# Optimization experiments

Measured on AMD Instinct MI355X. Metric: run time of the kernel, lower is better.

The kernel has to match this reference:

```python
import jax, jax.numpy as jnp
import numpy as np

N = 1_000_000   # total points
C = 20          # semantic classes
B = 4           # scenes in batch
L = 200         # instance label vocabulary
INST = 64       # number of proposals/instances
M = 300_000     # masked points (len(object_idxs))
T = 320_000     # total proposal rows
IGNORE = -100
PREPARE_EPOCHS = 128


def setup_inputs() -> dict:
    key = jax.random.key(0)
    ks = jax.random.split(key, 12)
    semantic_scores = jax.random.normal(ks[0], (N, C), jnp.float32)
    semantic_labels = jax.random.randint(ks[1], (N,), 0, C)
    lab = jax.random.randint(ks[2], (N,), 0, L)
    ign = jax.random.uniform(ks[3], (N,)) < 0.05
    instance_labels = jnp.where(ign, IGNORE, lab)
    pt_offsets = jax.random.normal(ks[4], (N, 3), jnp.float32)
    instance_info = jax.random.normal(ks[5], (N, 9), jnp.float32)
    coords = jax.random.normal(ks[6], (N, 3), jnp.float32)
    mask_logits = jax.random.normal(ks[7], (INST, M), jnp.float32)
    object_idxs = jax.random.randint(ks[8], (M,), 0, N)
    col1 = jax.random.randint(ks[9], (T,), 0, N)
    proposals_idx_shift = jnp.stack([jnp.zeros_like(col1), col1], axis=1)
    mids = jnp.sort(jax.random.randint(ks[10], (INST - 1,), 0, T))
    proposals_offset_shift = jnp.concatenate(
        [jnp.zeros((1,), jnp.int32), mids.astype(jnp.int32), jnp.full((1,), T, jnp.int32)])
    inst_batch_ids = jax.random.randint(ks[11], (INST,), 0, B)
    batch_offsets = jnp.array([0, N // 4, N // 2, 3 * N // 4, N], dtype=jnp.int32)
    batch_ids = jnp.clip(jnp.searchsorted(batch_offsets, object_idxs, side='right') - 1, 0, B - 1)
    inst_pred_seg_label = jax.random.randint(jax.random.fold_in(key, 99), (INST,), 0, C)
    return dict(semantic_scores=semantic_scores, pt_offsets=pt_offsets,
                instance_info=instance_info, coords=coords, mask_logits=mask_logits,
                semantic_labels=semantic_labels, instance_labels=instance_labels,
                object_idxs=object_idxs, proposals_idx_shift=proposals_idx_shift,
                proposals_offset_shift=proposals_offset_shift, inst_batch_ids=inst_batch_ids,
                batch_ids=batch_ids, batch_offsets=batch_offsets,
                inst_pred_seg_label=inst_pred_seg_label, epoch=200)


def reference(semantic_scores, pt_offsets, instance_info, coords, mask_logits,
              semantic_labels, instance_labels, object_idxs, proposals_idx_shift,
              proposals_offset_shift, inst_batch_ids, batch_ids, batch_offsets,
              inst_pred_seg_label, epoch):
    f32 = jnp.float32
    n_pts = semantic_scores.shape[0]
    n_inst, m_pts = mask_logits.shape
    n_batch = batch_offsets.shape[0] - 1
    LW = L + 1  # label buckets, bucket 0 == ignore(-100)

    # --- semantic cross entropy (ignore_index) ---
    logp = jax.nn.log_softmax(semantic_scores, axis=-1)
    sem_valid = semantic_labels != IGNORE
    safe_lab = jnp.where(sem_valid, semantic_labels, 0)
    nll = -jnp.take_along_axis(logp, safe_lab[:, None], axis=1)[:, 0]
    semantic_loss = jnp.sum(nll * sem_valid) / jnp.maximum(jnp.sum(sem_valid), 1)

    # --- offset losses ---
    gt_offsets = instance_info[:, 0:3] - coords
    pt_dist = jnp.sum(jnp.abs(pt_offsets - gt_offsets), axis=-1)
    valid = (instance_labels != IGNORE).astype(f32)
    vsum = jnp.sum(valid) + 1e-6
    offset_norm_loss = jnp.sum(pt_dist * valid) / vsum
    gt_u = gt_offsets / (jnp.linalg.norm(gt_offsets, axis=1, keepdims=True) + 1e-8)
    pt_u = pt_offsets / (jnp.linalg.norm(pt_offsets, axis=1, keepdims=True) + 1e-8)
    offset_dir_loss = jnp.sum(-jnp.sum(gt_u * pt_u, axis=-1) * valid) / vsum

    loss = semantic_loss + offset_norm_loss + offset_dir_loss

    if epoch > PREPARE_EPOCHS:
        # map instance labels to ids: ignore -> 0, label l -> l+1 (order-preserving, so
        # argmax-first tie-break == torch.mode smallest-value tie-break)
        labels_id = jnp.where(instance_labels == IGNORE, 0, instance_labels + 1)
        # segment id per proposal row from CSR offsets
        seg = jnp.clip(jnp.searchsorted(proposals_offset_shift, jnp.arange(T), side='right') - 1,
                       0, n_inst - 1)
        prop_lab = labels_id[proposals_idx_shift[:, 1]]
        hist = jax.ops.segment_sum(jnp.ones((T,), f32), seg * LW + prop_lab,
                                   num_segments=n_inst * LW).reshape(n_inst, LW)
        mode_id = jnp.argmax(hist, axis=1)                       # [INST] per-instance mode vote

        masked_lab = labels_id[object_idxs]                      # [M]
        sem_masked = semantic_labels[object_idxs]                # [M]
        skip = (mode_id == 0) | (inst_pred_seg_label <= 3)       # [INST]

        batch_match = inst_batch_ids[:, None] == batch_ids[None, :]           # [INST,M]
        sem_match = inst_pred_seg_label[:, None] == sem_masked[None, :]       # [INST,M]
        weights = batch_match.astype(f32) * jnp.where(skip[:, None], 1.0,
                                                      sem_match.astype(f32))  # [INST,M]

        # per-batch label histograms (full points and masked points)
        point_batch = jnp.clip(jnp.searchsorted(batch_offsets, jnp.arange(n_pts),
                                                side='right') - 1, 0, n_batch - 1)
        hist_full = jax.ops.segment_sum(jnp.ones((n_pts,), f32), point_batch * LW + labels_id,
                                        num_segments=n_batch * LW).reshape(n_batch, LW)
        hist_mask = jax.ops.segment_sum(jnp.ones((m_pts,), f32), batch_ids * LW + masked_lab,
                                        num_segments=n_batch * LW).reshape(n_batch, LW)
        num = hist_mask[inst_batch_ids, mode_id]
        den = hist_full[inst_batch_ids, mode_id]
        cover = jnp.where(den > 0, num / den, 0.0)
        pos = (~skip) & (cover > 0.3)
        inst_gt_mask = (pos[:, None] & (masked_lab[None, :] == mode_id[:, None])).astype(f32)

        pred = jax.nn.sigmoid(mask_logits)
        wb = (weights > 0).astype(f32)
        inter = jnp.sum(wb * pred * inst_gt_mask, axis=1)
        union = jnp.sum(wb * pred * pred, axis=1) + jnp.sum(wb * inst_gt_mask * inst_gt_mask, axis=1) + 1e-5
        dice_n = 1.0 - 2.0 * inter / union
        dice_valid = (~skip) & (jnp.sum(wb, axis=1) > 0)
        dice_loss = jnp.sum(jnp.where(dice_valid, dice_n, 0.0)) / (jnp.sum(dice_valid.astype(f32)) + 1e-6)

        # BCE(sigmoid(x), t) in stable form: softplus(x) - t*x
        bce = jax.nn.softplus(mask_logits) - inst_gt_mask * mask_logits
        score_loss = jnp.sum(bce * weights) / (jnp.sum(weights) + 1e-6)

        loss = loss + score_loss + dice_loss
    return loss
```

## Files before the change

### kernel.cpp

```cpp
#include <hip/hip_runtime.h>
#include <math.h>

namespace {

constexpr int N_PTS  = 1000000;
constexpr int C_CLS  = 20;
constexpr int N_B    = 4;
constexpr int L_LAB  = 200;
constexpr int LW     = L_LAB + 1;
constexpr int N_INST = 64;
constexpr int M_PTS  = 300000;
constexpr int T_PROP = 320000;
constexpr int IGN    = -100;
constexpr int PREP   = 128;

constexpr size_t OFF_G      = 0;
constexpr size_t OFF_INTER  = 64;
constexpr size_t OFF_UP     = 576;
constexpr size_t OFF_UG     = 1088;
constexpr size_t OFF_WBS    = 1600;
constexpr size_t OFF_SN     = 2112;
constexpr size_t OFF_HFULL  = 2624;
constexpr size_t OFF_HMASK  = 5840;
constexpr size_t OFF_IHIST  = 9056;
constexpr size_t OFF_FLAGS  = 60512;
constexpr size_t ZERO_BYTES = 60768;
constexpr size_t OFF_PART   = 60800;
constexpr size_t PART_BYTES = 5 * 1024 * 4;
constexpr size_t WS_PART_REQ = OFF_PART + PART_BYTES;
constexpr size_t OFF_META   = WS_PART_REQ;
constexpr size_t WS_REQUIRED = OFF_META + (size_t)M_PTS * 2;

__device__ __forceinline__ float waveSumF(float v) {
  #pragma unroll
  for (int off = 32; off > 0; off >>= 1) v += __shfl_down(v, off, 64);
  return v;
}
__device__ __forceinline__ int waveMaxI(int v) {
  #pragma unroll
  for (int off = 32; off > 0; off >>= 1) v = max(v, __shfl_down(v, off, 64));
  return v;
}

constexpr int PB_PT   = 1024;
constexpr int PB_HF   = 256;
constexpr int PB_PROP = 256;
constexpr int PB_HM   = 256;
constexpr int A_BLOCKS = PB_PT + PB_HF + PB_PROP + PB_HM;

constexpr int WREG = 560;

__global__ __launch_bounds__(256) void k_A(const float* __restrict__ scores,
                                           const float* __restrict__ pt_off,
                                           const float* __restrict__ info,
                                           const float* __restrict__ coords,
                                           const int* __restrict__ sem_lab,
                                           const int* __restrict__ inst_lab,
                                           const int* __restrict__ obj_idx,
                                           const int* __restrict__ batch_ids,
                                           const int* __restrict__ prop_idx,
                                           const int* __restrict__ prop_off,
                                           const int* __restrict__ batch_off,
                                           double* __restrict__ g,
                                           float* __restrict__ part,
                                           int use_part,
                                           int* __restrict__ hist_full,
                                           int* __restrict__ hist_mask,
                                           int* __restrict__ inst_hist,
                                           unsigned short* __restrict__ meta,
                                           int write_meta) {
  __shared__ float4 shbuf4[4 * WREG];
  int*   sh  = reinterpret_cast<int*>(shbuf4);
  float* shf = reinterpret_cast<float*>(shbuf4);
  const int bx = blockIdx.x;

  if (bx < PB_PT) {
    const int lane = threadIdx.x & 63, wv = threadIdx.x >> 6;
    float4* shw4 = shbuf4 + wv * WREG;
    float*  shwf = reinterpret_cast<float*>(shw4);
    float s_nll = 0.f, s_cnt = 0.f, s_dist = 0.f, s_dir = 0.f, s_val = 0.f;

    constexpr int NT      = N_PTS / 64;
    constexpr int TSTRIDE = PB_PT * 4;
    const int base = bx * 4 + wv;
    const int nit = (NT - bx * 4 + TSTRIDE - 1) / TSTRIDE;

    for (int it = 0; it < nit; ++it) {
      const int tile = base + it * TSTRIDE;
      if (tile < NT) {
        const int p = tile * 64 + lane;
        const int sl = sem_lab[p];
        const int il = inst_lab[p];

        const float4* s4 = reinterpret_cast<const float4*>(scores) + (size_t)tile * 320;
        #pragma unroll
        for (int r = 0; r < 5; ++r) shw4[r * 64 + lane] = s4[r * 64 + lane];
        const float4* c4 = reinterpret_cast<const float4*>(coords) + (size_t)tile * 48;
        const float4* o4 = reinterpret_cast<const float4*>(pt_off) + (size_t)tile * 48;
        const float4* i4 = reinterpret_cast<const float4*>(info)   + (size_t)tile * 144;
        if (lane < 48) { shw4[320 + lane] = c4[lane]; shw4[368 + lane] = o4[lane]; }
        shw4[416 + lane] = i4[lane];
        shw4[480 + lane] = i4[64 + lane];
        if (lane < 16) shw4[544 + lane] = i4[128 + lane];

        float mx = -3.4e38f;
        #pragma unroll
        for (int r = 0; r < 5; ++r) {
          const float4 a = shw4[lane * 5 + r];
          mx = fmaxf(mx, fmaxf(fmaxf(a.x, a.y), fmaxf(a.z, a.w)));
        }
        float se = 0.f;
        #pragma unroll
        for (int r = 0; r < 5; ++r) {
          const float4 a = shw4[lane * 5 + r];
          se += __expf(a.x - mx) + __expf(a.y - mx) + __expf(a.z - mx) + __expf(a.w - mx);
        }
        const float xs = shwf[lane * 20 + ((sl == IGN) ? 0 : sl)];
        if (sl != IGN) { s_nll += (mx + __logf(se)) - xs; s_cnt += 1.f; }

        if (il != IGN) {
          const float cx = shwf[1280 + 3 * lane + 0];
          const float cy = shwf[1280 + 3 * lane + 1];
          const float cz = shwf[1280 + 3 * lane + 2];
          const float ox = shwf[1472 + 3 * lane + 0];
          const float oy = shwf[1472 + 3 * lane + 1];
          const float oz = shwf[1472 + 3 * lane + 2];
          const float gx = shwf[1664 + 9 * lane + 0] - cx;
          const float gy = shwf[1664 + 9 * lane + 1] - cy;
          const float gz = shwf[1664 + 9 * lane + 2] - cz;
          s_val  += 1.f;
          s_dist += fabsf(ox - gx) + fabsf(oy - gy) + fabsf(oz - gz);
          const float gn = sqrtf(gx * gx + gy * gy + gz * gz) + 1e-8f;
          const float pn = sqrtf(ox * ox + oy * oy + oz * oz) + 1e-8f;
          s_dir += -((gx * ox + gy * oy + gz * oz) / (gn * pn));
        }
      }
    }

    __syncthreads();
    float vals[5] = { s_nll, s_cnt, s_dist, s_dir, s_val };
    #pragma unroll
    for (int k = 0; k < 5; ++k) {
      const float t = waveSumF(vals[k]);
      if (lane == 0) shf[k * 4 + wv] = t;
    }
    __syncthreads();
    if (threadIdx.x < 5) {
      const float s = shf[threadIdx.x * 4 + 0] + shf[threadIdx.x * 4 + 1] +
                      shf[threadIdx.x * 4 + 2] + shf[threadIdx.x * 4 + 3];
      if (use_part) part[threadIdx.x * PB_PT + bx] = s;
      else          atomicAdd(&g[threadIdx.x], (double)s);
    }
  } else if (bx < PB_PT + PB_HF) {
    for (int t = threadIdx.x; t < N_B * LW; t += blockDim.x) sh[t] = 0;
    __syncthreads();
    const int b1 = batch_off[1], b2 = batch_off[2], b3 = batch_off[3];
    const int blk = bx - PB_PT;
    const int4* il4p = reinterpret_cast<const int4*>(inst_lab);
    const int nq = N_PTS / 4;
    for (int q = blk * blockDim.x + threadIdx.x; q < nq; q += PB_HF * blockDim.x) {
      const int4 v = il4p[q];
      const int p = q * 4;
      const int ils[4] = { v.x, v.y, v.z, v.w };
      #pragma unroll
      for (int k = 0; k < 4; ++k) {
        const int lab = (ils[k] == IGN) ? 0 : (ils[k] + 1);
        const int pp = p + k;
        int pb = 0;
        if (pp >= b1) pb = 1;
        if (pp >= b2) pb = 2;
        if (pp >= b3) pb = 3;
        atomicAdd(&sh[pb * LW + lab], 1);
      }
    }
    __syncthreads();
    for (int t = threadIdx.x; t < N_B * LW; t += blockDim.x)
      if (sh[t]) atomicAdd(&hist_full[t], sh[t]);
  } else if (bx < PB_PT + PB_HF + PB_PROP) {
    if (threadIdx.x <= N_INST) sh[threadIdx.x] = prop_off[threadIdx.x];
    __syncthreads();
    const int blk = bx - PB_PT - PB_HF;
    const int4* pi4 = reinterpret_cast<const int4*>(prop_idx);
    const int nq = T_PROP / 2;
    for (int q = blk * blockDim.x + threadIdx.x; q < nq; q += PB_PROP * blockDim.x) {
      const int4 v = pi4[q];
      const int t0 = 2 * q, t1 = 2 * q + 1;
      const int il0 = inst_lab[v.y];
      const int il1 = inst_lab[v.w];
      int lo0 = 0, hi0 = N_INST + 1, lo1 = 0, hi1 = N_INST + 1;
      #pragma unroll
      for (int s = 0; s < 7; ++s) {
        const int m0 = (lo0 + hi0) >> 1;
        if (m0 <= N_INST && sh[m0] <= t0) lo0 = m0 + 1; else hi0 = m0;
        const int m1 = (lo1 + hi1) >> 1;
        if (m1 <= N_INST && sh[m1] <= t1) lo1 = m1 + 1; else hi1 = m1;
      }
      const int seg0 = min(lo0 - 1, N_INST - 1);
      const int seg1 = min(lo1 - 1, N_INST - 1);
      const int lab0 = (il0 == IGN) ? 0 : (il0 + 1);
      const int lab1 = (il1 == IGN) ? 0 : (il1 + 1);
      atomicAdd(&inst_hist[seg0 * LW + lab0], 1);
      atomicAdd(&inst_hist[seg1 * LW + lab1], 1);
    }
  } else {
    for (int t = threadIdx.x; t < N_B * LW; t += blockDim.x) sh[t] = 0;
    __syncthreads();
    const int blk = bx - PB_PT - PB_HF - PB_PROP;
    const int4* oi4 = reinterpret_cast<const int4*>(obj_idx);
    const int4* bi4 = reinterpret_cast<const int4*>(batch_ids);
    ushort4* m4 = reinterpret_cast<ushort4*>(meta);
    const int nq = M_PTS / 4;
    for (int q = blk * blockDim.x + threadIdx.x; q < nq; q += PB_HM * blockDim.x) {
      const int4 o = oi4[q];
      const int4 b = bi4[q];
      const int il0 = inst_lab[o.x], il1 = inst_lab[o.y],
                il2 = inst_lab[o.z], il3 = inst_lab[o.w];
      const int sm0 = sem_lab[o.x], sm1 = sem_lab[o.y],
                sm2 = sem_lab[o.z], sm3 = sem_lab[o.w];
      const int ml0 = (il0 == IGN) ? 0 : (il0 + 1);
      const int ml1 = (il1 == IGN) ? 0 : (il1 + 1);
      const int ml2 = (il2 == IGN) ? 0 : (il2 + 1);
      const int ml3 = (il3 == IGN) ? 0 : (il3 + 1);
      atomicAdd(&sh[b.x * LW + ml0], 1);
      atomicAdd(&sh[b.y * LW + ml1], 1);
      atomicAdd(&sh[b.z * LW + ml2], 1);
      atomicAdd(&sh[b.w * LW + ml3], 1);
      if (write_meta) {
        ushort4 mm;
        mm.x = (unsigned short)(ml0 | (sm0 << 8) | (b.x << 13));
        mm.y = (unsigned short)(ml1 | (sm1 << 8) | (b.y << 13));
        mm.z = (unsigned short)(ml2 | (sm2 << 8) | (b.z << 13));
        mm.w = (unsigned short)(ml3 | (sm3 << 8) | (b.w << 13));
        m4[q] = mm;
      }
    }
    __syncthreads();
    for (int t = threadIdx.x; t < N_B * LW; t += blockDim.x)
      if (sh[t]) atomicAdd(&hist_mask[t], sh[t]);
  }
}

__global__ __launch_bounds__(256) void k_argmax(const int* __restrict__ inst_hist,
                                                const int* __restrict__ hist_full,
                                                const int* __restrict__ hist_mask,
                                                const int* __restrict__ inst_batch_ids,
                                                const int* __restrict__ inst_seg,
                                                int* __restrict__ flags) {
  __shared__ int red[4];
  const int i = blockIdx.x;
  const int t = threadIdx.x;
  int key = 0;
  if (t < LW) {
    const int cnt = inst_hist[i * LW + t];
    key = (cnt << 8) | (255 - t);
  }
  key = waveMaxI(key);
  const int lane = t & 63, wv = t >> 6;
  if (lane == 0) red[wv] = key;
  __syncthreads();
  if (t == 0) {
    int k = max(max(red[0], red[1]), max(red[2], red[3]));
    const int m = 255 - (k & 0xFF);
    const int b = inst_batch_ids[i];
    const int seg = inst_seg[i];
    const bool skip = (m == 0) || (seg <= 3);
    const float num = (float)hist_mask[b * LW + m];
    const float den = (float)hist_full[b * LW + m];
    const float cover = (den > 0.f) ? (num / den) : 0.f;
    const bool pos = (!skip) && (cover > 0.3f);
    flags[i] = m | (skip ? 0x100 : 0) | (pos ? 0x200 : 0) | (b << 10) | (seg << 12);
  }
}

template <bool USE_META>
__global__ __launch_bounds__(256) void k_mask(const float* __restrict__ logits,
                                              const unsigned short* __restrict__ meta,
                                              const int* __restrict__ obj_idx,
                                              const int* __restrict__ inst_lab,
                                              const int* __restrict__ sem_lab,
                                              const int* __restrict__ batch_ids,
                                              const int* __restrict__ flags,
                                              double* __restrict__ i_inter,
                                              double* __restrict__ i_up,
                                              double* __restrict__ i_ug,
                                              double* __restrict__ i_wbs,
                                              double* __restrict__ i_sn) {
  const int i  = blockIdx.y;
  const int fl = flags[i];
  const int  mode_i = fl & 0xFF;
  const bool skip   = (fl >> 8) & 1;
  const bool pos    = (fl >> 9) & 1;
  const int  bi     = (fl >> 10) & 3;
  const int  seg    = (fl >> 12) & 31;

  float inter = 0.f, up = 0.f, ug = 0.f, wbs = 0.f, sn = 0.f;

  if (USE_META) {
    const float4* row4 = reinterpret_cast<const float4*>(logits + (size_t)i * M_PTS);
    const ushort4* m4  = reinterpret_cast<const ushort4*>(meta);
    const int nq = M_PTS / 4;
    for (int q = blockIdx.x * blockDim.x + threadIdx.x; q < nq; q += gridDim.x * blockDim.x) {
      const float4  x4 = row4[q];
      const ushort4 d4 = m4[q];
      const float xs[4] = { x4.x, x4.y, x4.z, x4.w };
      const int   ds[4] = { d4.x, d4.y, d4.z, d4.w };
      #pragma unroll
      for (int k = 0; k < 4; ++k) {
        const int md = ds[k];
        const int ml = md & 0xFF;
        const int sm = (md >> 8) & 31;
        const int b  = (md >> 13) & 3;
        const bool w  = (b == bi) && (skip || (sm == seg));
        const bool gt = pos && (ml == mode_i);
        const float x  = xs[k];
        const float e  = __expf(-fabsf(x));
        const float r  = __builtin_amdgcn_rcpf(1.f + e);
        const float pr = (x >= 0.f) ? r : e * r;
        const float sp = fmaxf(x, 0.f) + __logf(1.f + e);
        const float wf = w ? 1.f : 0.f;
        const float gf = gt ? 1.f : 0.f;
        up    += wf * pr * pr;
        wbs   += wf;
        sn    += wf * (sp - gf * x);
        inter += wf * gf * pr;
        ug    += wf * gf;
      }
    }
  } else {
    const float* row = logits + (size_t)i * M_PTS;
    for (int j = blockIdx.x * blockDim.x + threadIdx.x; j < M_PTS; j += gridDim.x * blockDim.x) {
      const int o  = obj_idx[j];
      const int il = inst_lab[o];
      const int ml = (il == IGN) ? 0 : (il + 1);
      const int sm = sem_lab[o];
      const int b  = batch_ids[j];
      const bool w  = (b == bi) && (skip || (sm == seg));
      const bool gt = pos && (ml == mode_i);
      const float x  = row[j];
      const float e  = __expf(-fabsf(x));
      const float r  = __builtin_amdgcn_rcpf(1.f + e);
      const float pr = (x >= 0.f) ? r : e * r;
      const float sp = fmaxf(x, 0.f) + __logf(1.f + e);
      const float wf = w ? 1.f : 0.f;
      const float gf = gt ? 1.f : 0.f;
      up    += wf * pr * pr;
      wbs   += wf;
      sn    += wf * (sp - gf * x);
      inter += wf * gf * pr;
      ug    += wf * gf;
    }
  }

  __shared__ float red[5][4];
  float vals[5] = { inter, up, ug, wbs, sn };
  const int lane = threadIdx.x & 63, wv = threadIdx.x >> 6;
  #pragma unroll
  for (int k = 0; k < 5; ++k) {
    const float t = waveSumF(vals[k]);
    if (lane == 0) red[k][wv] = t;
  }
  __syncthreads();
  if (threadIdx.x < 5) {
    const float s = red[threadIdx.x][0] + red[threadIdx.x][1] + red[threadIdx.x][2] + red[threadIdx.x][3];
    double* dst = (threadIdx.x == 0) ? (i_inter + i)
                : (threadIdx.x == 1) ? (i_up + i)
                : (threadIdx.x == 2) ? (i_ug + i)
                : (threadIdx.x == 3) ? (i_wbs + i)
                                     : (i_sn + i);
    atomicAdd(dst, (double)s);
  }
}

__global__ __launch_bounds__(256) void k_final(const double* __restrict__ g,
                                               const float* __restrict__ part,
                                               int use_part,
                                               const double* __restrict__ i_inter,
                                               const double* __restrict__ i_up,
                                               const double* __restrict__ i_ug,
                                               const double* __restrict__ i_wbs,
                                               const double* __restrict__ i_sn,
                                               const int* __restrict__ flags,
                                               const int* __restrict__ epoch,
                                               float* __restrict__ out) {
  __shared__ double sred[5][4];
  __shared__ double sG[5];
  __shared__ double sI[4];
  const int t = threadIdx.x, lane = t & 63, wv = t >> 6;

  if (use_part) {
    #pragma unroll
    for (int c = 0; c < 5; ++c) {
      double v = 0.0;
      #pragma unroll
      for (int j = 0; j < 4; ++j) v += (double)part[c * 1024 + t + j * 256];
      #pragma unroll
      for (int off = 32; off > 0; off >>= 1) v += __shfl_down(v, off, 64);
      if (lane == 0) sred[c][wv] = v;
    }
    __syncthreads();
    if (t < 5) sG[t] = sred[t][0] + sred[t][1] + sred[t][2] + sred[t][3];
  } else {
    if (t < 5) sG[t] = g[t];
  }

  const bool act = epoch[0] > PREP;
  if (t < 64) {
    double sn = 0.0, wsum = 0.0, dice = 0.0, dcnt = 0.0;
    if (act) {
      wsum = i_wbs[t];
      sn   = i_sn[t];
      const bool skip = (flags[t] >> 8) & 1;
      if (!skip && wsum > 0.0) {
        const double un = i_up[t] + i_ug[t] + 1e-5;
        dice = 1.0 - 2.0 * i_inter[t] / un;
        dcnt = 1.0;
      }
      #pragma unroll
      for (int off = 32; off > 0; off >>= 1) {
        wsum += __shfl_down(wsum, off, 64);
        sn   += __shfl_down(sn,   off, 64);
        dice += __shfl_down(dice, off, 64);
        dcnt += __shfl_down(dcnt, off, 64);
      }
    }
    if (t == 0) { sI[0] = sn; sI[1] = wsum; sI[2] = dice; sI[3] = dcnt; }
  }
  __syncthreads();
  if (t == 0) {
    double loss = sG[0] / fmax(sG[1], 1.0);
    const double vsum = sG[4] + 1e-6;
    loss += sG[2] / vsum + sG[3] / vsum;
    if (act) loss += sI[0] / (sI[1] + 1e-6) + sI[2] / (sI[3] + 1e-6);
    out[0] = (float)loss;
  }
}

}

extern "C" void kernel_launch(void* const* d_in, const int* in_sizes, int n_in,
                              void* d_out, int out_size, void* d_ws, size_t ws_size,
                              hipStream_t stream) {
  const float* semantic_scores  = (const float*)d_in[0];
  const float* pt_offsets       = (const float*)d_in[1];
  const float* instance_info    = (const float*)d_in[2];
  const float* coords           = (const float*)d_in[3];
  const float* mask_logits      = (const float*)d_in[4];
  const int*   semantic_labels  = (const int*)d_in[5];
  const int*   instance_labels  = (const int*)d_in[6];
  const int*   object_idxs      = (const int*)d_in[7];
  const int*   proposals_idx    = (const int*)d_in[8];
  const int*   proposals_off    = (const int*)d_in[9];
  const int*   inst_batch_ids   = (const int*)d_in[10];
  const int*   batch_ids        = (const int*)d_in[11];
  const int*   batch_offsets    = (const int*)d_in[12];
  const int*   inst_seg         = (const int*)d_in[13];
  const int*   epoch            = (const int*)d_in[14];
  float* out = (float*)d_out;

  char* w = (char*)d_ws;
  double* g        = (double*)(w + OFF_G);
  double* i_inter  = (double*)(w + OFF_INTER);
  double* i_up     = (double*)(w + OFF_UP);
  double* i_ug     = (double*)(w + OFF_UG);
  double* i_wbs    = (double*)(w + OFF_WBS);
  double* i_sn     = (double*)(w + OFF_SN);
  int* hist_full   = (int*)(w + OFF_HFULL);
  int* hist_mask   = (int*)(w + OFF_HMASK);
  int* inst_hist   = (int*)(w + OFF_IHIST);
  int* flags       = (int*)(w + OFF_FLAGS);
  float* part      = (float*)(w + OFF_PART);
  unsigned short* meta = (unsigned short*)(w + OFF_META);

  const bool use_part = (ws_size >= WS_PART_REQ);
  const bool use_meta = (ws_size >= WS_REQUIRED);

  (void)hipMemsetAsync(d_ws, 0, ZERO_BYTES, stream);

  k_A<<<A_BLOCKS, 256, 0, stream>>>(semantic_scores, pt_offsets, instance_info, coords,
                                    semantic_labels, instance_labels, object_idxs,
                                    batch_ids, proposals_idx, proposals_off, batch_offsets,
                                    g, part, use_part ? 1 : 0,
                                    hist_full, hist_mask, inst_hist, meta,
                                    use_meta ? 1 : 0);

  k_argmax<<<N_INST, 256, 0, stream>>>(inst_hist, hist_full, hist_mask,
                                       inst_batch_ids, inst_seg, flags);

  dim3 mgrid(40, N_INST);
  if (use_meta) {
    k_mask<true><<<mgrid, 256, 0, stream>>>(mask_logits, meta, object_idxs, instance_labels,
                                            semantic_labels, batch_ids, flags,
                                            i_inter, i_up, i_ug, i_wbs, i_sn);
  } else {
    k_mask<false><<<mgrid, 256, 0, stream>>>(mask_logits, meta, object_idxs, instance_labels,
                                             semantic_labels, batch_ids, flags,
                                             i_inter, i_up, i_ug, i_wbs, i_sn);
  }
  k_final<<<1, 256, 0, stream>>>(g, part, use_part ? 1 : 0,
                                 i_inter, i_up, i_ug, i_wbs, i_sn, flags, epoch, out);
}
```

Measured before the change: 293.4 us.

## Software-prefetch point tiles into registers and unroll mask-row loads by two

```diff
diff --git a/kernel.cpp b/kernel.cpp
--- a/kernel.cpp
+++ b/kernel.cpp
@@ -42,39 +42,72 @@
   return v;
 }
 
-constexpr int PB_PT   = 1024;
 constexpr int PB_HF   = 256;
 constexpr int PB_PROP = 256;
 constexpr int PB_HM   = 256;
-constexpr int A_BLOCKS = PB_PT + PB_HF + PB_PROP + PB_HM;
+constexpr int PB_PT   = 1024;
+constexpr int PT_BASE = PB_HF + PB_PROP + PB_HM;
+constexpr int A_BLOCKS = PT_BASE + PB_PT;
 
 constexpr int WREG = 560;
 
-__global__ __launch_bounds__(256) void k_A(const float* __restrict__ scores,
-                                           const float* __restrict__ pt_off,
-                                           const float* __restrict__ info,
-                                           const float* __restrict__ coords,
-                                           const int* __restrict__ sem_lab,
-                                           const int* __restrict__ inst_lab,
-                                           const int* __restrict__ obj_idx,
-                                           const int* __restrict__ batch_ids,
-                                           const int* __restrict__ prop_idx,
-                                           const int* __restrict__ prop_off,
-                                           const int* __restrict__ batch_off,
-                                           double* __restrict__ g,
-                                           float* __restrict__ part,
-                                           int use_part,
-                                           int* __restrict__ hist_full,
-                                           int* __restrict__ hist_mask,
-                                           int* __restrict__ inst_hist,
-                                           unsigned short* __restrict__ meta,
-                                           int write_meta) {
+struct PtRegs {
+  float4 r0, r1, r2, r3, r4;
+  float4 rc, ro;
+  float4 ri0, ri1, ri2;
+  int sl, il;
+};
+
+__device__ __forceinline__ void pt_load(PtRegs& R, int tile, int lane,
+                                        const float4* __restrict__ s4b,
+                                        const float4* __restrict__ c4b,
+                                        const float4* __restrict__ o4b,
+                                        const float4* __restrict__ i4b,
+                                        const int* __restrict__ sem_lab,
+                                        const int* __restrict__ inst_lab) {
+  const float4* s4 = s4b + (size_t)tile * 320;
+  R.r0 = s4[lane];
+  R.r1 = s4[64 + lane];
+  R.r2 = s4[128 + lane];
+  R.r3 = s4[192 + lane];
+  R.r4 = s4[256 + lane];
+  const float4* c4 = c4b + (size_t)tile * 48;
+  const float4* o4 = o4b + (size_t)tile * 48;
+  const float4* i4 = i4b + (size_t)tile * 144;
+  if (lane < 48) { R.rc = c4[lane]; R.ro = o4[lane]; }
+  R.ri0 = i4[lane];
+  R.ri1 = i4[64 + lane];
+  if (lane < 16) R.ri2 = i4[128 + lane];
+  const int p = tile * 64 + lane;
+  R.sl = sem_lab[p];
+  R.il = inst_lab[p];
+}
+
+__global__ __launch_bounds__(256, 4) void k_A(const float* __restrict__ scores,
+                                              const float* __restrict__ pt_off,
+                                              const float* __restrict__ info,
+                                              const float* __restrict__ coords,
+                                              const int* __restrict__ sem_lab,
+                                              const int* __restrict__ inst_lab,
+                                              const int* __restrict__ obj_idx,
+                                              const int* __restrict__ batch_ids,
+                                              const int* __restrict__ prop_idx,
+                                              const int* __restrict__ prop_off,
+                                              const int* __restrict__ batch_off,
+                                              double* __restrict__ g,
+                                              float* __restrict__ part,
+                                              int use_part,
+                                              int* __restrict__ hist_full,
+                                              int* __restrict__ hist_mask,
+                                              int* __restrict__ inst_hist,
+                                              unsigned short* __restrict__ meta,
+                                              int write_meta) {
   __shared__ float4 shbuf4[4 * WREG];
   int*   sh  = reinterpret_cast<int*>(shbuf4);
   float* shf = reinterpret_cast<float*>(shbuf4);
   const int bx = blockIdx.x;
 
-  if (bx < PB_PT) {
+  if (bx >= PT_BASE) {
     const int lane = threadIdx.x & 63, wv = threadIdx.x >> 6;
     float4* shw4 = shbuf4 + wv * WREG;
     float*  shwf = reinterpret_cast<float*>(shw4);
@@ -82,27 +115,39 @@
 
     constexpr int NT      = N_PTS / 64;
     constexpr int TSTRIDE = PB_PT * 4;
-    const int base = bx * 4 + wv;
-    const int nit = (NT - bx * 4 + TSTRIDE - 1) / TSTRIDE;
+    const int bxp  = bx - PT_BASE;
+    const int base = bxp * 4 + wv;
+    const int nit  = (NT - bxp * 4 + TSTRIDE - 1) / TSTRIDE;
+
+    const float4* s4b = reinterpret_cast<const float4*>(scores);
+    const float4* c4b = reinterpret_cast<const float4*>(coords);
+    const float4* o4b = reinterpret_cast<const float4*>(pt_off);
+    const float4* i4b = reinterpret_cast<const float4*>(info);
+
+    PtRegs R;
+    int tile = base;
+    if (tile < NT) pt_load(R, tile, lane, s4b, c4b, o4b, i4b, sem_lab, inst_lab);
 
     for (int it = 0; it < nit; ++it) {
-      const int tile = base + it * TSTRIDE;
-      if (tile < NT) {
-        const int p = tile * 64 + lane;
-        const int sl = sem_lab[p];
-        const int il = inst_lab[p];
-
-        const float4* s4 = reinterpret_cast<const float4*>(scores) + (size_t)tile * 320;
-        #pragma unroll
-        for (int r = 0; r < 5; ++r) shw4[r * 64 + lane] = s4[r * 64 + lane];
-        const float4* c4 = reinterpret_cast<const float4*>(coords) + (size_t)tile * 48;
-        const float4* o4 = reinterpret_cast<const float4*>(pt_off) + (size_t)tile * 48;
-        const float4* i4 = reinterpret_cast<const float4*>(info)   + (size_t)tile * 144;
-        if (lane < 48) { shw4[320 + lane] = c4[lane]; shw4[368 + lane] = o4[lane]; }
-        shw4[416 + lane] = i4[lane];
-        shw4[480 + lane] = i4[64 + lane];
-        if (lane < 16) shw4[544 + lane] = i4[128 + lane];
-
+      const int cur = tile;
+      const int nxt = tile + TSTRIDE;
+      const int sl = R.sl, il = R.il;
+
+      if (cur < NT) {
+        shw4[lane]        = R.r0;
+        shw4[64 + lane]   = R.r1;
+        shw4[128 + lane]  = R.r2;
+        shw4[192 + lane]  = R.r3;
+        shw4[256 + lane]  = R.r4;
+        if (lane < 48) { shw4[320 + lane] = R.rc; shw4[368 + lane] = R.ro; }
+        shw4[416 + lane]  = R.ri0;
+        shw4[480 + lane]  = R.ri1;
+        if (lane < 16) shw4[544 + lane] = R.ri2;
+      }
+
+      if (nxt < NT) pt_load(R, nxt, lane, s4b, c4b, o4b, i4b, sem_lab, inst_lab);
+
+      if (cur < NT) {
         float mx = -3.4e38f;
         #pragma unroll
         for (int r = 0; r < 5; ++r) {
@@ -135,6 +180,7 @@
           s_dir += -((gx * ox + gy * oy + gz * oz) / (gn * pn));
         }
       }
+      tile = nxt;
     }
 
     __syncthreads();
@@ -148,14 +194,14 @@
     if (threadIdx.x < 5) {
       const float s = shf[threadIdx.x * 4 + 0] + shf[threadIdx.x * 4 + 1] +
                       shf[threadIdx.x * 4 + 2] + shf[threadIdx.x * 4 + 3];
-      if (use_part) part[threadIdx.x * PB_PT + bx] = s;
+      if (use_part) part[threadIdx.x * PB_PT + bxp] = s;
       else          atomicAdd(&g[threadIdx.x], (double)s);
     }
-  } else if (bx < PB_PT + PB_HF) {
+  } else if (bx < PB_HF) {
     for (int t = threadIdx.x; t < N_B * LW; t += blockDim.x) sh[t] = 0;
     __syncthreads();
     const int b1 = batch_off[1], b2 = batch_off[2], b3 = batch_off[3];
-    const int blk = bx - PB_PT;
+    const int blk = bx;
     const int4* il4p = reinterpret_cast<const int4*>(inst_lab);
     const int nq = N_PTS / 4;
     for (int q = blk * blockDim.x + threadIdx.x; q < nq; q += PB_HF * blockDim.x) {
@@ -176,10 +222,10 @@
     __syncthreads();
     for (int t = threadIdx.x; t < N_B * LW; t += blockDim.x)
       if (sh[t]) atomicAdd(&hist_full[t], sh[t]);
-  } else if (bx < PB_PT + PB_HF + PB_PROP) {
+  } else if (bx < PB_HF + PB_PROP) {
     if (threadIdx.x <= N_INST) sh[threadIdx.x] = prop_off[threadIdx.x];
     __syncthreads();
-    const int blk = bx - PB_PT - PB_HF;
+    const int blk = bx - PB_HF;
     const int4* pi4 = reinterpret_cast<const int4*>(prop_idx);
     const int nq = T_PROP / 2;
     for (int q = blk * blockDim.x + threadIdx.x; q < nq; q += PB_PROP * blockDim.x) {
@@ -205,7 +251,7 @@
   } else {
     for (int t = threadIdx.x; t < N_B * LW; t += blockDim.x) sh[t] = 0;
     __syncthreads();
-    const int blk = bx - PB_PT - PB_HF - PB_PROP;
+    const int blk = bx - PB_HF - PB_PROP;
     const int4* oi4 = reinterpret_cast<const int4*>(obj_idx);
     const int4* bi4 = reinterpret_cast<const int4*>(batch_ids);
     ushort4* m4 = reinterpret_cast<ushort4*>(meta);
@@ -295,37 +341,47 @@
 
   float inter = 0.f, up = 0.f, ug = 0.f, wbs = 0.f, sn = 0.f;
 
+  auto acc4 = [&](const float4& x4, const ushort4& d4) {
+    const float xs[4] = { x4.x, x4.y, x4.z, x4.w };
+    const int   ds[4] = { d4.x, d4.y, d4.z, d4.w };
+    #pragma unroll
+    for (int k = 0; k < 4; ++k) {
+      const int md = ds[k];
+      const int ml = md & 0xFF;
+      const int sm = (md >> 8) & 31;
+      const int b  = (md >> 13) & 3;
+      const bool w  = (b == bi) && (skip || (sm == seg));
+      const bool gt = pos && (ml == mode_i);
+      const float x  = xs[k];
+      const float e  = __expf(-fabsf(x));
+      const float r  = __builtin_amdgcn_rcpf(1.f + e);
+      const float pr = (x >= 0.f) ? r : e * r;
+      const float sp = fmaxf(x, 0.f) + __logf(1.f + e);
+      const float wf = w ? 1.f : 0.f;
+      const float gf = gt ? 1.f : 0.f;
+      up    += wf * pr * pr;
+      wbs   += wf;
+      sn    += wf * (sp - gf * x);
+      inter += wf * gf * pr;
+      ug    += wf * gf;
+    }
+  };
+
   if (USE_META) {
     const float4* row4 = reinterpret_cast<const float4*>(logits + (size_t)i * M_PTS);
     const ushort4* m4  = reinterpret_cast<const ushort4*>(meta);
     const int nq = M_PTS / 4;
-    for (int q = blockIdx.x * blockDim.x + threadIdx.x; q < nq; q += gridDim.x * blockDim.x) {
-      const float4  x4 = row4[q];
-      const ushort4 d4 = m4[q];
-      const float xs[4] = { x4.x, x4.y, x4.z, x4.w };
-      const int   ds[4] = { d4.x, d4.y, d4.z, d4.w };
-      #pragma unroll
-      for (int k = 0; k < 4; ++k) {
-        const int md = ds[k];
-        const int ml = md & 0xFF;
-        const int sm = (md >> 8) & 31;
-        const int b  = (md >> 13) & 3;
-        const bool w  = (b == bi) && (skip || (sm == seg));
-        const bool gt = pos && (ml == mode_i);
-        const float x  = xs[k];
-        const float e  = __expf(-fabsf(x));
-        const float r  = __builtin_amdgcn_rcpf(1.f + e);
-        const float pr = (x >= 0.f) ? r : e * r;
-        const float sp = fmaxf(x, 0.f) + __logf(1.f + e);
-        const float wf = w ? 1.f : 0.f;
-        const float gf = gt ? 1.f : 0.f;
-        up    += wf * pr * pr;
-        wbs   += wf;
-        sn    += wf * (sp - gf * x);
-        inter += wf * gf * pr;
-        ug    += wf * gf;
-      }
-    }
+    const int stride = gridDim.x * blockDim.x;
+    int q = blockIdx.x * blockDim.x + threadIdx.x;
+    for (; q + stride < nq; q += 2 * stride) {
+      const float4  xa = row4[q];
+      const ushort4 da = m4[q];
+      const float4  xb = row4[q + stride];
+      const ushort4 db = m4[q + stride];
+      acc4(xa, da);
+      acc4(xb, db);
+    }
+    for (; q < nq; q += stride) acc4(row4[q], m4[q]);
   } else {
     const float* row = logits + (size_t)i * M_PTS;
     for (int j = blockIdx.x * blockDim.x + threadIdx.x; j < M_PTS; j += gridDim.x * blockDim.x) {
```

Result: slower. 317.5 us (+8.2%).

## Move point-loss pass into mask kernel and fold argmax into per-block prologue

Applied to the files above, without the earlier changes.

```diff
diff --git a/kernel.cpp b/kernel.cpp
--- a/kernel.cpp
+++ b/kernel.cpp
@@ -13,6 +13,19 @@
 constexpr int T_PROP = 320000;
 constexpr int IGN    = -100;
 constexpr int PREP   = 128;
+
+constexpr int GB_HF   = 256;
+constexpr int GB_PROP = 256;
+constexpr int GB_HM   = 256;
+constexpr int G_BLOCKS = GB_HF + GB_PROP + GB_HM;
+
+constexpr int JB_PT   = 2048;
+constexpr int JB_MK   = 2048;
+constexpr int J_BLOCKS = JB_PT + JB_MK;
+constexpr int NT       = N_PTS / 64;
+constexpr int PT_WAVES = JB_PT * 4;
+constexpr int MK_PER_I = JB_MK / N_INST;
+constexpr int MSTRIDE  = MK_PER_I * 256;
 
 constexpr size_t OFF_G      = 0;
 constexpr size_t OFF_INTER  = 64;
@@ -26,7 +39,7 @@
 constexpr size_t OFF_FLAGS  = 60512;
 constexpr size_t ZERO_BYTES = 60768;
 constexpr size_t OFF_PART   = 60800;
-constexpr size_t PART_BYTES = 5 * 1024 * 4;
+constexpr size_t PART_BYTES = 5 * (size_t)JB_PT * 4;
 constexpr size_t WS_PART_REQ = OFF_PART + PART_BYTES;
 constexpr size_t OFF_META   = WS_PART_REQ;
 constexpr size_t WS_REQUIRED = OFF_META + (size_t)M_PTS * 2;
@@ -42,123 +55,28 @@
   return v;
 }
 
-constexpr int PB_PT   = 1024;
-constexpr int PB_HF   = 256;
-constexpr int PB_PROP = 256;
-constexpr int PB_HM   = 256;
-constexpr int A_BLOCKS = PB_PT + PB_HF + PB_PROP + PB_HM;
-
-constexpr int WREG = 560;
-
-__global__ __launch_bounds__(256) void k_A(const float* __restrict__ scores,
-                                           const float* __restrict__ pt_off,
-                                           const float* __restrict__ info,
-                                           const float* __restrict__ coords,
-                                           const int* __restrict__ sem_lab,
-                                           const int* __restrict__ inst_lab,
-                                           const int* __restrict__ obj_idx,
-                                           const int* __restrict__ batch_ids,
-                                           const int* __restrict__ prop_idx,
-                                           const int* __restrict__ prop_off,
-                                           const int* __restrict__ batch_off,
-                                           double* __restrict__ g,
-                                           float* __restrict__ part,
-                                           int use_part,
-                                           int* __restrict__ hist_full,
-                                           int* __restrict__ hist_mask,
-                                           int* __restrict__ inst_hist,
-                                           unsigned short* __restrict__ meta,
-                                           int write_meta) {
-  __shared__ float4 shbuf4[4 * WREG];
-  int*   sh  = reinterpret_cast<int*>(shbuf4);
-  float* shf = reinterpret_cast<float*>(shbuf4);
+__global__ __launch_bounds__(256) void k_gather(const int* __restrict__ sem_lab,
+                                                const int* __restrict__ inst_lab,
+                                                const int* __restrict__ obj_idx,
+                                                const int* __restrict__ batch_ids,
+                                                const int* __restrict__ prop_idx,
+                                                const int* __restrict__ prop_off,
+                                                const int* __restrict__ batch_off,
+                                                int* __restrict__ hist_full,
+                                                int* __restrict__ hist_mask,
+                                                int* __restrict__ inst_hist,
+                                                unsigned short* __restrict__ meta,
+                                                int write_meta) {
+  __shared__ int sh[N_B * LW];
   const int bx = blockIdx.x;
 
-  if (bx < PB_PT) {
-    const int lane = threadIdx.x & 63, wv = threadIdx.x >> 6;
-    float4* shw4 = shbuf4 + wv * WREG;
-    float*  shwf = reinterpret_cast<float*>(shw4);
-    float s_nll = 0.f, s_cnt = 0.f, s_dist = 0.f, s_dir = 0.f, s_val = 0.f;
-
-    constexpr int NT      = N_PTS / 64;
-    constexpr int TSTRIDE = PB_PT * 4;
-    const int base = bx * 4 + wv;
-    const int nit = (NT - bx * 4 + TSTRIDE - 1) / TSTRIDE;
-
-    for (int it = 0; it < nit; ++it) {
-      const int tile = base + it * TSTRIDE;
-      if (tile < NT) {
-        const int p = tile * 64 + lane;
-        const int sl = sem_lab[p];
-        const int il = inst_lab[p];
-
-        const float4* s4 = reinterpret_cast<const float4*>(scores) + (size_t)tile * 320;
-        #pragma unroll
-        for (int r = 0; r < 5; ++r) shw4[r * 64 + lane] = s4[r * 64 + lane];
-        const float4* c4 = reinterpret_cast<const float4*>(coords) + (size_t)tile * 48;
-        const float4* o4 = reinterpret_cast<const float4*>(pt_off) + (size_t)tile * 48;
-        const float4* i4 = reinterpret_cast<const float4*>(info)   + (size_t)tile * 144;
-        if (lane < 48) { shw4[320 + lane] = c4[lane]; shw4[368 + lane] = o4[lane]; }
-        shw4[416 + lane] = i4[lane];
-        shw4[480 + lane] = i4[64 + lane];
-        if (lane < 16) shw4[544 + lane] = i4[128 + lane];
-
-        float mx = -3.4e38f;
-        #pragma unroll
-        for (int r = 0; r < 5; ++r) {
-          const float4 a = shw4[lane * 5 + r];
-          mx = fmaxf(mx, fmaxf(fmaxf(a.x, a.y), fmaxf(a.z, a.w)));
-        }
-        float se = 0.f;
-        #pragma unroll
-        for (int r = 0; r < 5; ++r) {
-          const float4 a = shw4[lane * 5 + r];
-          se += __expf(a.x - mx) + __expf(a.y - mx) + __expf(a.z - mx) + __expf(a.w - mx);
-        }
-        const float xs = shwf[lane * 20 + ((sl == IGN) ? 0 : sl)];
-        if (sl != IGN) { s_nll += (mx + __logf(se)) - xs; s_cnt += 1.f; }
-
-        if (il != IGN) {
-          const float cx = shwf[1280 + 3 * lane + 0];
-          const float cy = shwf[1280 + 3 * lane + 1];
-          const float cz = shwf[1280 + 3 * lane + 2];
-          const float ox = shwf[1472 + 3 * lane + 0];
-          const float oy = shwf[1472 + 3 * lane + 1];
-          const float oz = shwf[1472 + 3 * lane + 2];
-          const float gx = shwf[1664 + 9 * lane + 0] - cx;
-          const float gy = shwf[1664 + 9 * lane + 1] - cy;
-          const float gz = shwf[1664 + 9 * lane + 2] - cz;
-          s_val  += 1.f;
-          s_dist += fabsf(ox - gx) + fabsf(oy - gy) + fabsf(oz - gz);
-          const float gn = sqrtf(gx * gx + gy * gy + gz * gz) + 1e-8f;
-          const float pn = sqrtf(ox * ox + oy * oy + oz * oz) + 1e-8f;
-          s_dir += -((gx * ox + gy * oy + gz * oz) / (gn * pn));
-        }
-      }
-    }
-
-    __syncthreads();
-    float vals[5] = { s_nll, s_cnt, s_dist, s_dir, s_val };
-    #pragma unroll
-    for (int k = 0; k < 5; ++k) {
-      const float t = waveSumF(vals[k]);
-      if (lane == 0) shf[k * 4 + wv] = t;
-    }
-    __syncthreads();
-    if (threadIdx.x < 5) {
-      const float s = shf[threadIdx.x * 4 + 0] + shf[threadIdx.x * 4 + 1] +
-                      shf[threadIdx.x * 4 + 2] + shf[threadIdx.x * 4 + 3];
-      if (use_part) part[threadIdx.x * PB_PT + bx] = s;
-      else          atomicAdd(&g[threadIdx.x], (double)s);
-    }
-  } else if (bx < PB_PT + PB_HF) {
+  if (bx < GB_HF) {
     for (int t = threadIdx.x; t < N_B * LW; t += blockDim.x) sh[t] = 0;
     __syncthreads();
     const int b1 = batch_off[1], b2 = batch_off[2], b3 = batch_off[3];
-    const int blk = bx - PB_PT;
     const int4* il4p = reinterpret_cast<const int4*>(inst_lab);
     const int nq = N_PTS / 4;
-    for (int q = blk * blockDim.x + threadIdx.x; q < nq; q += PB_HF * blockDim.x) {
+    for (int q = bx * blockDim.x + threadIdx.x; q < nq; q += GB_HF * blockDim.x) {
       const int4 v = il4p[q];
       const int p = q * 4;
       const int ils[4] = { v.x, v.y, v.z, v.w };
@@ -176,13 +94,13 @@
     __syncthreads();
     for (int t = threadIdx.x; t < N_B * LW; t += blockDim.x)
       if (sh[t]) atomicAdd(&hist_full[t], sh[t]);
-  } else if (bx < PB_PT + PB_HF + PB_PROP) {
+  } else if (bx < GB_HF + GB_PROP) {
     if (threadIdx.x <= N_INST) sh[threadIdx.x] = prop_off[threadIdx.x];
     __syncthreads();
-    const int blk = bx - PB_PT - PB_HF;
+    const int blk = bx - GB_HF;
     const int4* pi4 = reinterpret_cast<const int4*>(prop_idx);
     const int nq = T_PROP / 2;
-    for (int q = blk * blockDim.x + threadIdx.x; q < nq; q += PB_PROP * blockDim.x) {
+    for (int q = blk * blockDim.x + threadIdx.x; q < nq; q += GB_PROP * blockDim.x) {
       const int4 v = pi4[q];
       const int t0 = 2 * q, t1 = 2 * q + 1;
       const int il0 = inst_lab[v.y];
@@ -205,12 +123,12 @@
   } else {
     for (int t = threadIdx.x; t < N_B * LW; t += blockDim.x) sh[t] = 0;
     __syncthreads();
-    const int blk = bx - PB_PT - PB_HF - PB_PROP;
+    const int blk = bx - GB_HF - GB_PROP;
     const int4* oi4 = reinterpret_cast<const int4*>(obj_idx);
     const int4* bi4 = reinterpret_cast<const int4*>(batch_ids);
     ushort4* m4 = reinterpret_cast<ushort4*>(meta);
     const int nq = M_PTS / 4;
-    for (int q = blk * blockDim.x + threadIdx.x; q < nq; q += PB_HM * blockDim.x) {
+    for (int q = blk * blockDim.x + threadIdx.x; q < nq; q += GB_HM * blockDim.x) {
       const int4 o = oi4[q];
       const int4 b = bi4[q];
       const int il0 = inst_lab[o.x], il1 = inst_lab[o.y],
@@ -240,79 +158,157 @@
   }
 }
 
-__global__ __launch_bounds__(256) void k_argmax(const int* __restrict__ inst_hist,
-                                                const int* __restrict__ hist_full,
-                                                const int* __restrict__ hist_mask,
-                                                const int* __restrict__ inst_batch_ids,
-                                                const int* __restrict__ inst_seg,
-                                                int* __restrict__ flags) {
-  __shared__ int red[4];
-  const int i = blockIdx.x;
-  const int t = threadIdx.x;
-  int key = 0;
-  if (t < LW) {
-    const int cnt = inst_hist[i * LW + t];
-    key = (cnt << 8) | (255 - t);
-  }
-  key = waveMaxI(key);
-  const int lane = t & 63, wv = t >> 6;
-  if (lane == 0) red[wv] = key;
-  __syncthreads();
-  if (t == 0) {
-    int k = max(max(red[0], red[1]), max(red[2], red[3]));
-    const int m = 255 - (k & 0xFF);
-    const int b = inst_batch_ids[i];
-    const int seg = inst_seg[i];
-    const bool skip = (m == 0) || (seg <= 3);
-    const float num = (float)hist_mask[b * LW + m];
-    const float den = (float)hist_full[b * LW + m];
-    const float cover = (den > 0.f) ? (num / den) : 0.f;
-    const bool pos = (!skip) && (cover > 0.3f);
-    flags[i] = m | (skip ? 0x100 : 0) | (pos ? 0x200 : 0) | (b << 10) | (seg << 12);
-  }
-}
-
 template <bool USE_META>
-__global__ __launch_bounds__(256) void k_mask(const float* __restrict__ logits,
-                                              const unsigned short* __restrict__ meta,
-                                              const int* __restrict__ obj_idx,
-                                              const int* __restrict__ inst_lab,
-                                              const int* __restrict__ sem_lab,
-                                              const int* __restrict__ batch_ids,
-                                              const int* __restrict__ flags,
-                                              double* __restrict__ i_inter,
-                                              double* __restrict__ i_up,
-                                              double* __restrict__ i_ug,
-                                              double* __restrict__ i_wbs,
-                                              double* __restrict__ i_sn) {
-  const int i  = blockIdx.y;
-  const int fl = flags[i];
-  const int  mode_i = fl & 0xFF;
-  const bool skip   = (fl >> 8) & 1;
-  const bool pos    = (fl >> 9) & 1;
-  const int  bi     = (fl >> 10) & 3;
-  const int  seg    = (fl >> 12) & 31;
-
-  float inter = 0.f, up = 0.f, ug = 0.f, wbs = 0.f, sn = 0.f;
-
-  if (USE_META) {
-    const float4* row4 = reinterpret_cast<const float4*>(logits + (size_t)i * M_PTS);
-    const ushort4* m4  = reinterpret_cast<const ushort4*>(meta);
-    const int nq = M_PTS / 4;
-    for (int q = blockIdx.x * blockDim.x + threadIdx.x; q < nq; q += gridDim.x * blockDim.x) {
-      const float4  x4 = row4[q];
-      const ushort4 d4 = m4[q];
-      const float xs[4] = { x4.x, x4.y, x4.z, x4.w };
-      const int   ds[4] = { d4.x, d4.y, d4.z, d4.w };
+__global__ __launch_bounds__(256, 8) void k_joint(const float* __restrict__ scores,
+                                                  const float* __restrict__ pt_off,
+                                                  const float* __restrict__ info,
+                                                  const float* __restrict__ coords,
+                                                  const int* __restrict__ sem_lab,
+                                                  const int* __restrict__ inst_lab,
+                                                  const int* __restrict__ obj_idx,
+                                                  const int* __restrict__ batch_ids,
+                                                  const float* __restrict__ logits,
+                                                  const unsigned short* __restrict__ meta,
+                                                  const int* __restrict__ inst_hist,
+                                                  const int* __restrict__ hist_full,
+                                                  const int* __restrict__ hist_mask,
+                                                  const int* __restrict__ inst_batch_ids,
+                                                  const int* __restrict__ inst_seg,
+                                                  int* __restrict__ flags,
+                                                  double* __restrict__ g,
+                                                  float* __restrict__ part,
+                                                  int use_part,
+                                                  double* __restrict__ i_inter,
+                                                  double* __restrict__ i_up,
+                                                  double* __restrict__ i_ug,
+                                                  double* __restrict__ i_wbs,
+                                                  double* __restrict__ i_sn) {
+  __shared__ float4 shbuf4[4 * 320];
+  float* shf = reinterpret_cast<float*>(shbuf4);
+  int*   shi = reinterpret_cast<int*>(shbuf4);
+  const int bx = blockIdx.x;
+  const int lane = threadIdx.x & 63, wv = threadIdx.x >> 6;
+
+  if (bx < JB_PT) {
+    float4* shw4 = shbuf4 + wv * 320;
+    float*  shwf = reinterpret_cast<float*>(shw4);
+    float s_nll = 0.f, s_cnt = 0.f, s_dist = 0.f, s_dir = 0.f, s_val = 0.f;
+
+    const int wgid = bx * 4 + wv;
+    const float4* s4b = reinterpret_cast<const float4*>(scores);
+    const float4* c4b = reinterpret_cast<const float4*>(coords);
+    const float4* o4b = reinterpret_cast<const float4*>(pt_off);
+    const float4* i4b = reinterpret_cast<const float4*>(info);
+
+    for (int tile = wgid; tile < NT; tile += PT_WAVES) {
+      const int p = tile * 64 + lane;
+      const int sl = sem_lab[p];
+      const int il = inst_lab[p];
+
+      const float4* s4 = s4b + (size_t)tile * 320;
+      #pragma unroll
+      for (int r = 0; r < 5; ++r) shw4[r * 64 + lane] = s4[r * 64 + lane];
+
+      float mx = -3.4e38f;
+      #pragma unroll
+      for (int r = 0; r < 5; ++r) {
+        const float4 a = shw4[lane * 5 + r];
+        mx = fmaxf(mx, fmaxf(fmaxf(a.x, a.y), fmaxf(a.z, a.w)));
+      }
+      float se = 0.f;
+      #pragma unroll
+      for (int r = 0; r < 5; ++r) {
+        const float4 a = shw4[lane * 5 + r];
+        se += __expf(a.x - mx) + __expf(a.y - mx) + __expf(a.z - mx) + __expf(a.w - mx);
+      }
+      const float xs = shwf[lane * 20 + ((sl == IGN) ? 0 : sl)];
+      if (sl != IGN) { s_nll += (mx + __logf(se)) - xs; s_cnt += 1.f; }
+
+      const float4* c4 = c4b + (size_t)tile * 48;
+      const float4* o4 = o4b + (size_t)tile * 48;
+      const float4* i4 = i4b + (size_t)tile * 144;
+      if (lane < 48) { shw4[lane] = c4[lane]; shw4[48 + lane] = o4[lane]; }
+      shw4[96 + lane]  = i4[lane];
+      shw4[160 + lane] = i4[64 + lane];
+      if (lane < 16) shw4[224 + lane] = i4[128 + lane];
+
+      if (il != IGN) {
+        const float cx = shwf[3 * lane + 0], cy = shwf[3 * lane + 1], cz = shwf[3 * lane + 2];
+        const float ox = shwf[192 + 3 * lane + 0], oy = shwf[192 + 3 * lane + 1], oz = shwf[192 + 3 * lane + 2];
+        const float gx = shwf[384 + 9 * lane + 0] - cx;
+        const float gy = shwf[384 + 9 * lane + 1] - cy;
+        const float gz = shwf[384 + 9 * lane + 2] - cz;
+        s_val  += 1.f;
+        s_dist += fabsf(ox - gx) + fabsf(oy - gy) + fabsf(oz - gz);
+        const float gn = sqrtf(gx * gx + gy * gy + gz * gz) + 1e-8f;
+        const float pn = sqrtf(ox * ox + oy * oy + oz * oz) + 1e-8f;
+        s_dir += -((gx * ox + gy * oy + gz * oz) / (gn * pn));
+      }
+    }
+
+    __syncthreads();
+    float vals[5] = { s_nll, s_cnt, s_dist, s_dir, s_val };
+    #pragma unroll
+    for (int k = 0; k < 5; ++k) {
+      const float t = waveSumF(vals[k]);
+      if (lane == 0) shf[k * 4 + wv] = t;
+    }
+    __syncthreads();
+    if (threadIdx.x < 5) {
+      const float s = shf[threadIdx.x * 4 + 0] + shf[threadIdx.x * 4 + 1] +
+                      shf[threadIdx.x * 4 + 2] + shf[threadIdx.x * 4 + 3];
+      if (use_part) part[threadIdx.x * JB_PT + bx] = s;
+      else          atomicAdd(&g[threadIdx.x], (double)s);
+    }
+  } else {
+    const int bx2 = bx - JB_PT;
+    const int i  = bx2 >> 5;
+    const int xp = bx2 & (MK_PER_I - 1);
+
+    {
+      const int t = threadIdx.x;
+      int key = 0;
+      if (t < LW) key = (inst_hist[i * LW + t] << 8) | (255 - t);
+      key = waveMaxI(key);
+      if ((t & 63) == 0) shi[32 + (t >> 6)] = key;
+      __syncthreads();
+      if (t == 0) {
+        const int k = max(max(shi[32], shi[33]), max(shi[34], shi[35]));
+        const int m = 255 - (k & 0xFF);
+        const int b = inst_batch_ids[i];
+        const int seg = inst_seg[i];
+        const bool skip = (m == 0) || (seg <= 3);
+        const float num = (float)hist_mask[b * LW + m];
+        const float den = (float)hist_full[b * LW + m];
+        const float cover = (den > 0.f) ? (num / den) : 0.f;
+        const bool pos = (!skip) && (cover > 0.3f);
+        const int fl = m | (skip ? 0x100 : 0) | (pos ? 0x200 : 0) | (b << 10) | (seg << 12);
+        shi[36] = fl;
+        if (xp == 0) flags[i] = fl;
+      }
+      __syncthreads();
+    }
+    const int fl = shi[36];
+    const int  mode_i = fl & 0xFF;
+    const bool skip   = (fl >> 8) & 1;
+    const bool pos    = (fl >> 9) & 1;
+    const int  bi     = (fl >> 10) & 3;
+    const int  seg    = (fl >> 12) & 31;
+
+    float inter = 0.f, up = 0.f, ug = 0.f, wbs = 0.f, sn = 0.f;
+
+    auto acc4 = [&](const float4& x4, const ushort4& d4) {
+      const float xsv[4] = { x4.x, x4.y, x4.z, x4.w };
+      const int   dsv[4] = { d4.x, d4.y, d4.z, d4.w };
       #pragma unroll
       for (int k = 0; k < 4; ++k) {
-        const int md = ds[k];
+        const int md = dsv[k];
         const int ml = md & 0xFF;
         const int sm = (md >> 8) & 31;
         const int b  = (md >> 13) & 3;
         const bool w  = (b == bi) && (skip || (sm == seg));
         const bool gt = pos && (ml == mode_i);
-        const float x  = xs[k];
+        const float x  = xsv[k];
         const float e  = __expf(-fabsf(x));
         const float r  = __builtin_amdgcn_rcpf(1.f + e);
         const float pr = (x >= 0.f) ? r : e * r;
@@ -325,49 +321,65 @@
         inter += wf * gf * pr;
         ug    += wf * gf;
       }
-    }
-  } else {
-    const float* row = logits + (size_t)i * M_PTS;
-    for (int j = blockIdx.x * blockDim.x + threadIdx.x; j < M_PTS; j += gridDim.x * blockDim.x) {
-      const int o  = obj_idx[j];
-      const int il = inst_lab[o];
-      const int ml = (il == IGN) ? 0 : (il + 1);
-      const int sm = sem_lab[o];
-      const int b  = batch_ids[j];
-      const bool w  = (b == bi) && (skip || (sm == seg));
-      const bool gt = pos && (ml == mode_i);
-      const float x  = row[j];
-      const float e  = __expf(-fabsf(x));
-      const float r  = __builtin_amdgcn_rcpf(1.f + e);
-      const float pr = (x >= 0.f) ? r : e * r;
-      const float sp = fmaxf(x, 0.f) + __logf(1.f + e);
-      const float wf = w ? 1.f : 0.f;
-      const float gf = gt ? 1.f : 0.f;
-      up    += wf * pr * pr;
-      wbs   += wf;
-      sn    += wf * (sp - gf * x);
-      inter += wf * gf * pr;
-      ug    += wf * gf;
-    }
-  }
-
-  __shared__ float red[5][4];
-  float vals[5] = { inter, up, ug, wbs, sn };
-  const int lane = threadIdx.x & 63, wv = threadIdx.x >> 6;
-  #pragma unroll
-  for (int k = 0; k < 5; ++k) {
-    const float t = waveSumF(vals[k]);
-    if (lane == 0) red[k][wv] = t;
-  }
-  __syncthreads();
-  if (threadIdx.x < 5) {
-    const float s = red[threadIdx.x][0] + red[threadIdx.x][1] + red[threadIdx.x][2] + red[threadIdx.x][3];
-    double* dst = (threadIdx.x == 0) ? (i_inter + i)
-                : (threadIdx.x == 1) ? (i_up + i)
-                : (threadIdx.x == 2) ? (i_ug + i)
-                : (threadIdx.x == 3) ? (i_wbs + i)
-                                     : (i_sn + i);
-    atomicAdd(dst, (double)s);
+    };
+
+    if (USE_META) {
+      const float4* row4 = reinterpret_cast<const float4*>(logits + (size_t)i * M_PTS);
+      const ushort4* m4  = reinterpret_cast<const ushort4*>(meta);
+      const int nq = M_PTS / 4;
+      int q = xp * 256 + threadIdx.x;
+      for (; q + MSTRIDE < nq; q += 2 * MSTRIDE) {
+        const float4  xa = row4[q];
+        const ushort4 da = m4[q];
+        const float4  xb = row4[q + MSTRIDE];
+        const ushort4 db = m4[q + MSTRIDE];
+        acc4(xa, da);
+        acc4(xb, db);
+      }
+      for (; q < nq; q += MSTRIDE) acc4(row4[q], m4[q]);
+    } else {
+      const float* row = logits + (size_t)i * M_PTS;
+      for (int j = xp * 256 + threadIdx.x; j < M_PTS; j += MSTRIDE) {
+        const int o  = obj_idx[j];
+        const int il = inst_lab[o];
+        const int ml = (il == IGN) ? 0 : (il + 1);
+        const int sm = sem_lab[o];
+        const int b  = batch_ids[j];
+        const bool w  = (b == bi) && (skip || (sm == seg));
+        const bool gt = pos && (ml == mode_i);
+        const float x  = row[j];
+        const float e  = __expf(-fabsf(x));
+        const float r  = __builtin_amdgcn_rcpf(1.f + e);
+        const float pr = (x >= 0.f) ? r : e * r;
+        const float sp = fmaxf(x, 0.f) + __logf(1.f + e);
+        const float wf = w ? 1.f : 0.f;
+        const float gf = gt ? 1.f : 0.f;
+        up    += wf * pr * pr;
+        wbs   += wf;
+        sn    += wf * (sp - gf * x);
+        inter += wf * gf * pr;
+        ug    += wf * gf;
+      }
+    }
+
+    __syncthreads();
+    float vals[5] = { inter, up, ug, wbs, sn };
+    #pragma unroll
+    for (int k = 0; k < 5; ++k) {
+      const float t = waveSumF(vals[k]);
+      if (lane == 0) shf[k * 4 + wv] = t;
+    }
+    __syncthreads();
+    if (threadIdx.x < 5) {
+      const float s = shf[threadIdx.x * 4 + 0] + shf[threadIdx.x * 4 + 1] +
+                      shf[threadIdx.x * 4 + 2] + shf[threadIdx.x * 4 + 3];
+      double* dst = (threadIdx.x == 0) ? (i_inter + i)
+                  : (threadIdx.x == 1) ? (i_up + i)
+                  : (threadIdx.x == 2) ? (i_ug + i)
+                  : (threadIdx.x == 3) ? (i_wbs + i)
+                                       : (i_sn + i);
+      atomicAdd(dst, (double)s);
+    }
   }
 }
 
@@ -392,7 +404,7 @@
     for (int c = 0; c < 5; ++c) {
       double v = 0.0;
       #pragma unroll
-      for (int j = 0; j < 4; ++j) v += (double)part[c * 1024 + t + j * 256];
+      for (int j = 0; j < 8; ++j) v += (double)part[c * JB_PT + t + j * 256];
       #pragma unroll
       for (int off = 32; off > 0; off >>= 1) v += __shfl_down(v, off, 64);
       if (lane == 0) sred[c][wv] = v;
@@ -476,26 +488,29 @@
 
   (void)hipMemsetAsync(d_ws, 0, ZERO_BYTES, stream);
 
-  k_A<<<A_BLOCKS, 256, 0, stream>>>(semantic_scores, pt_offsets, instance_info, coords,
-                                    semantic_labels, instance_labels, object_idxs,
-                                    batch_ids, proposals_idx, proposals_off, batch_offsets,
-                                    g, part, use_part ? 1 : 0,
-                                    hist_full, hist_mask, inst_hist, meta,
-                                    use_meta ? 1 : 0);
-
-  k_argmax<<<N_INST, 256, 0, stream>>>(inst_hist, hist_full, hist_mask,
-                                       inst_batch_ids, inst_seg, flags);
-
-  dim3 mgrid(40, N_INST);
+  k_gather<<<G_BLOCKS, 256, 0, stream>>>(semantic_labels, instance_labels, object_idxs,
+                                         batch_ids, proposals_idx, proposals_off,
+                                         batch_offsets, hist_full, hist_mask, inst_hist,
+                                         meta, use_meta ? 1 : 0);
+
   if (use_meta) {
-    k_mask<true><<<mgrid, 256, 0, stream>>>(mask_logits, meta, object_idxs, instance_labels,
-                                            semantic_labels, batch_ids, flags,
-                                            i_inter, i_up, i_ug, i_wbs, i_sn);
+    k_joint<true><<<J_BLOCKS, 256, 0, stream>>>(semantic_scores, pt_offsets, instance_info,
+                                                coords, semantic_labels, instance_labels,
+                                                object_idxs, batch_ids, mask_logits, meta,
+                                                inst_hist, hist_full, hist_mask,
+                                                inst_batch_ids, inst_seg, flags,
+                                                g, part, use_part ? 1 : 0,
+                                                i_inter, i_up, i_ug, i_wbs, i_sn);
   } else {
-    k_mask<false><<<mgrid, 256, 0, stream>>>(mask_logits, meta, object_idxs, instance_labels,
-                                             semantic_labels, batch_ids, flags,
-                                             i_inter, i_up, i_ug, i_wbs, i_sn);
+    k_joint<false><<<J_BLOCKS, 256, 0, stream>>>(semantic_scores, pt_offsets, instance_info,
+                                                 coords, semantic_labels, instance_labels,
+                                                 object_idxs, batch_ids, mask_logits, meta,
+                                                 inst_hist, hist_full, hist_mask,
+                                                 inst_batch_ids, inst_seg, flags,
+                                                 g, part, use_part ? 1 : 0,
+                                                 i_inter, i_up, i_ug, i_wbs, i_sn);
   }
+
   k_final<<<1, 256, 0, stream>>>(g, part, use_part ? 1 : 0,
                                  i_inter, i_up, i_ug, i_wbs, i_sn, flags, epoch, out);
 }
```

Result: no change. 297.0 us (+1.3%).
